# Optimization experiments

Hardware: AMD Instinct MI355X
Metric: run time of the kernel (lower is better)

## Reference

```python
import jax, jax.numpy as jnp
import numpy as np

N_NODES = 10000
N_EDGES = 160000
HID = 128
N_LAYERS = 6
N_RBF = 50
CUTOFF = 10.0
EDGE_IN = 2 * HID + N_RBF + 1  # 307


def setup_inputs() -> dict:
    key = jax.random.key(0)
    ks = jax.random.split(key, 24)
    s = 0.05
    inp = {
        'atomic_numbers': jax.random.randint(ks[0], (N_NODES,), 0, 100),
        'coords': jax.random.normal(ks[1], (N_NODES, 3), jnp.float32),
        'edge_index': jax.random.randint(ks[2], (2, N_EDGES), 0, N_NODES),
        'embed': jax.random.normal(ks[3], (100, HID), jnp.float32) * s,
        # message_net (stacked over layers)
        'mw1': jax.random.normal(ks[4], (N_LAYERS, EDGE_IN, HID), jnp.float32) * s,
        'mb1': jnp.zeros((N_LAYERS, HID), jnp.float32),
        'mw2': jax.random.normal(ks[5], (N_LAYERS, HID, HID), jnp.float32) * s,
        'mb2': jnp.zeros((N_LAYERS, HID), jnp.float32),
        # coord_net
        'cw1': jax.random.normal(ks[6], (N_LAYERS, HID, HID), jnp.float32) * s,
        'cb1': jnp.zeros((N_LAYERS, HID), jnp.float32),
        'cw2': jax.random.normal(ks[7], (N_LAYERS, HID, 1), jnp.float32) * s,
        'cb2': jnp.zeros((N_LAYERS, 1), jnp.float32),
        # feature_net
        'fw': jax.random.normal(ks[8], (N_LAYERS, 2 * HID, HID), jnp.float32) * s,
        'fb': jnp.zeros((N_LAYERS, HID), jnp.float32),
        # energy_predictor
        'ew1': jax.random.normal(ks[9], (HID, HID), jnp.float32) * s,
        'eb1': jnp.zeros((HID,), jnp.float32),
        'ew2': jax.random.normal(ks[10], (HID, 1), jnp.float32) * s,
        'eb2': jnp.zeros((1,), jnp.float32),
    }
    return inp


def _forward(atomic_numbers, coords, edge_index, embed,
             mw1, mb1, mw2, mb2, cw1, cb1, cw2, cb2, fw, fb,
             ew1, eb1, ew2, eb2):
    silu = jax.nn.silu
    n = coords.shape[0]
    row, col = edge_index[0], edge_index[1]
    feats = embed[atomic_numbers]                    # [N, H]
    # RBF edge attributes (computed once from initial coords)
    d = jnp.linalg.norm(coords[row] - coords[col], axis=-1)[:, None]  # [E,1]
    centers = jnp.linspace(0.0, CUTOFF, N_RBF)
    width = CUTOFF / N_RBF
    rbf = jnp.exp(-((d - centers) ** 2) / width)
    cut = 0.5 * (jnp.cos(jnp.pi * d / CUTOFF) + 1.0) * (d < CUTOFF).astype(d.dtype)
    edge_attr = rbf * cut                            # [E, 50]
    for l in range(N_LAYERS):
        diff = coords[row] - coords[col]             # [E, 3]
        edist = jnp.sum(diff * diff, axis=-1, keepdims=True)  # squared dist, [E,1]
        ef = jnp.concatenate([feats[row], feats[col], edist, edge_attr], axis=-1)
        m = silu(silu(ef @ mw1[l] + mb1[l]) @ mw2[l] + mb2[l])        # [E, H]
        w = silu(m @ cw1[l] + cb1[l]) @ cw2[l] + cb2[l]               # [E, 1]
        coords = coords.at[row].add(w * diff)                         # equivariant coord update
        agg = jax.ops.segment_sum(m, row, num_segments=n)             # [N, H]
        feats = silu(jnp.concatenate([feats, agg], axis=-1) @ fw[l] + fb[l])
    atom_e = silu(feats @ ew1 + eb1) @ ew2 + eb2     # [N, 1]
    return jnp.sum(atom_e)


def reference(atomic_numbers, coords, edge_index, embed,
              mw1, mb1, mw2, mb2, cw1, cb1, cw2, cb2, fw, fb,
              ew1, eb1, ew2, eb2):
    return _forward(atomic_numbers, coords, edge_index, embed,
                    mw1, mb1, mw2, mb2, cw1, cb1, cw2, cb2, fw, fb,
                    ew1, eb1, ew2, eb2)
```

## Files before the change

kernel.cpp:

```cpp
#include <hip/hip_runtime.h>
#include <math.h>

#define N_NODES  10000
#define N_EDGES  160000
#define HID      128
#define N_LAYERS 6
#define N_RBF    50
#define EDGE_IN  307
#define KP1      320
#define M_TILE   64
#define N_TILES  (N_EDGES / M_TILE)

typedef short bf16x8 __attribute__((ext_vector_type(8)));
typedef float f32x4  __attribute__((ext_vector_type(4)));

__device__ __forceinline__ float silu_f(float x) {
    return x / (1.0f + __expf(-x));
}
__device__ __forceinline__ short f2bf(float f) {
    union { float f; unsigned u; } v; v.f = f;
    unsigned r = v.u + 0x7FFFu + ((v.u >> 16) & 1u);
    return (short)(r >> 16);
}
__device__ __forceinline__ float bf2f(unsigned short s) {
    union { float f; unsigned u; } v; v.u = ((unsigned)s) << 16;
    return v.f;
}


__global__ void init_feats_kernel(const int* __restrict__ an,
                                  const float* __restrict__ embed,
                                  short* __restrict__ featsB) {
    int idx = blockIdx.x * blockDim.x + threadIdx.x;
    if (idx < N_NODES * HID) {
        int i = idx >> 7, j = idx & 127;
        featsB[idx] = f2bf(embed[an[i] * HID + j]);
    }
}

__global__ void hist_kernel(const int* __restrict__ row, int* __restrict__ cnt) {
    int e = blockIdx.x * blockDim.x + threadIdx.x;
    if (e < N_EDGES) atomicAdd(&cnt[row[e]], 1);
}

__global__ void scan_kernel(const int* __restrict__ cnt, int* __restrict__ cursor) {
    __shared__ int buf[256];
    __shared__ int carry;
    int tid = threadIdx.x;
    if (tid == 0) carry = 0;
    __syncthreads();
    for (int base = 0; base < N_NODES; base += 256) {
        int v = (base + tid < N_NODES) ? cnt[base + tid] : 0;
        buf[tid] = v;
        __syncthreads();
        for (int off = 1; off < 256; off <<= 1) {
            int x = (tid >= off) ? buf[tid - off] : 0;
            __syncthreads();
            buf[tid] += x;
            __syncthreads();
        }
        int excl = buf[tid] - v + carry;
        if (base + tid < N_NODES) cursor[base + tid] = excl;
        int tot = buf[255];
        __syncthreads();
        if (tid == 0) carry += tot;
        __syncthreads();
    }
}

__global__ void scatter_kernel(const int* __restrict__ row, int* __restrict__ cursor,
                               int* __restrict__ sorted) {
    int e = blockIdx.x * blockDim.x + threadIdx.x;
    if (e < N_EDGES) {
        int p = atomicAdd(&cursor[row[e]], 1);
        sorted[p] = e;
    }
}

__global__ void edgegeom_kernel(const int* __restrict__ sorted,
                                const int* __restrict__ erow, const int* __restrict__ ecol,
                                const float* __restrict__ coords,
                                float* __restrict__ d0, float* __restrict__ cut0) {
    int p = blockIdx.x * 256 + threadIdx.x;
    if (p < N_EDGES) {
        int e = sorted[p];
        int r = erow[e], c = ecol[e];
        float dx = coords[3*r]   - coords[3*c];
        float dy = coords[3*r+1] - coords[3*c+1];
        float dz = coords[3*r+2] - coords[3*c+2];
        float d = sqrtf(dx*dx + dy*dy + dz*dz);
        d0[p] = d;
        cut0[p] = (d < 10.0f) ? 0.5f * (__cosf(0.31415926535f * d) + 1.0f) : 0.0f;
    }
}

#define WT_L (40960 + 16384 + 16384 + 32768)
__global__ void wtrans_kernel(const float* __restrict__ mw1, const float* __restrict__ mw2,
                              const float* __restrict__ cw1, const float* __restrict__ fw,
                              short* __restrict__ wtm1, short* __restrict__ wtm2,
                              short* __restrict__ wtc1, short* __restrict__ wtf) {
    int idx = blockIdx.x * blockDim.x + threadIdx.x;
    if (idx >= N_LAYERS * WT_L) return;
    int l = idx / WT_L;
    int r = idx - l * WT_L;
    if (r < 40960) {
        int n = r / KP1, k = r - n * KP1;
        float v = (k < EDGE_IN) ? mw1[(size_t)l * EDGE_IN * HID + (size_t)k * HID + n] : 0.f;
        wtm1[(size_t)l * 40960 + r] = f2bf(v);
    } else if ((r -= 40960) < 16384) {
        int n = r >> 7, k = r & 127;
        wtm2[(size_t)l * 16384 + r] = f2bf(mw2[(size_t)l * HID * HID + (size_t)k * HID + n]);
    } else if ((r -= 16384) < 16384) {
        int n = r >> 7, k = r & 127;
        wtc1[(size_t)l * 16384 + r] = f2bf(cw1[(size_t)l * HID * HID + (size_t)k * HID + n]);
    } else {
        r -= 16384;
        int n = r >> 8, k = r & 255;
        wtf[(size_t)l * 32768 + r] = f2bf(fw[(size_t)l * 2 * HID * HID + (size_t)k * HID + n]);
    }
}


#define SMEM_BYTES 18432

__global__ __launch_bounds__(256) void edge_kernel(
    const int* __restrict__ sorted,
    const int* __restrict__ erow, const int* __restrict__ ecol,
    const float* __restrict__ coords, float* __restrict__ coords_next,
    const short* __restrict__ featsB,
    const float* __restrict__ d0g, const float* __restrict__ cut0g,
    const short* __restrict__ wtm1, const float* __restrict__ mb1,
    const short* __restrict__ wtm2, const float* __restrict__ mb2,
    const short* __restrict__ wtc1, const float* __restrict__ cb1,
    const float* __restrict__ cw2, const float* __restrict__ cb2,
    float* __restrict__ agg)
{
    __shared__ char  smem[SMEM_BYTES];
    __shared__ int   srow[M_TILE];
    __shared__ int   scol[M_TILE];
    __shared__ float sdiff[M_TILE][3];
    __shared__ float sdist[M_TILE], sd0[M_TILE], scut[M_TILE], sW[M_TILE];
    __shared__ float sWp[M_TILE][4];
    __shared__ float sB1[HID], sB2[HID], sC1[HID], sV[HID];

    short (*sA)[64][72] = (short (*)[64][72])smem;
    short (*sH)[136]    = (short (*)[136])smem;

    const int tid = threadIdx.x;
    const int p0 = blockIdx.x * M_TILE;
    const int wave = tid >> 6, lane = tid & 63, quad = lane >> 4, lm = lane & 15;
    const int el = tid >> 2, kq = (tid & 3) * 16;
    const int colA = wave * 32 + lm, colB = colA + 16;

    if (tid < M_TILE) {
        int e = sorted[p0 + tid];
        int r = erow[e], c = ecol[e];
        srow[tid] = r; scol[tid] = c;
        float dx = coords[3*r]   - coords[3*c];
        float dy = coords[3*r+1] - coords[3*c+1];
        float dz = coords[3*r+2] - coords[3*c+2];
        sdiff[tid][0] = dx; sdiff[tid][1] = dy; sdiff[tid][2] = dz;
        sdist[tid] = dx*dx + dy*dy + dz*dz;
        sd0[tid]  = d0g[p0 + tid];
        scut[tid] = cut0g[p0 + tid];
    }
    if (tid < HID) {
        sB1[tid] = mb1[tid]; sB2[tid] = mb2[tid];
        sC1[tid] = cb1[tid]; sV[tid]  = cw2[tid];
    }
    const float cb2v = cb2[0];
    __syncthreads();

    f32x4 acc[4][2];
    #pragma unroll
    for (int mt = 0; mt < 4; ++mt) { acc[mt][0] = (f32x4)0.f; acc[mt][1] = (f32x4)0.f; }

    bf16x8 bwb[2][2][2];
    {
        int node = srow[el];
        const bf16x8* src = (const bf16x8*)&featsB[(size_t)node * HID + kq];
        bf16x8 a0 = src[0], a1 = src[1];
        #pragma unroll
        for (int h = 0; h < 2; ++h) {
            bwb[0][h][0] = *(const bf16x8*)&wtm1[(size_t)colA * KP1 + h * 32 + quad * 8];
            bwb[0][h][1] = *(const bf16x8*)&wtm1[(size_t)colB * KP1 + h * 32 + quad * 8];
        }
        *(bf16x8*)&sA[0][el][kq]     = a0;
        *(bf16x8*)&sA[0][el][kq + 8] = a1;
    }
    __syncthreads();
    #pragma unroll
    for (int c = 0; c < 5; ++c) {
        bf16x8 a0, a1;
        if (c < 3) {
            int node = (c + 1 < 2) ? srow[el] : scol[el];
            const bf16x8* src =
                (const bf16x8*)&featsB[(size_t)node * HID + ((c + 1) & 1) * 64 + kq];
            a0 = src[0]; a1 = src[1];
        } else if (c == 3) {
            float dv = sd0[el], ct = scut[el], ds2 = sdist[el];
            #pragma unroll
            for (int j = 0; j < 8; ++j) {
                int k = 256 + kq + j;
                float v = 0.f;
                if (k == 256) v = ds2;
                else if (k < EDGE_IN) {
                    float cen = (float)(k - 257) * (10.0f / 49.0f);
                    float t = dv - cen;
                    v = __expf(-t * t * 5.0f) * ct;
                }
                a0[j] = f2bf(v);
            }
            #pragma unroll
            for (int j = 0; j < 8; ++j) {
                int k = 264 + kq + j;
                float v = 0.f;
                if (k < EDGE_IN) {
                    float cen = (float)(k - 257) * (10.0f / 49.0f);
                    float t = dv - cen;
                    v = __expf(-t * t * 5.0f) * ct;
                }
                a1[j] = f2bf(v);
            }
        }
        if (c < 4) {
            int k1 = (c + 1) * 64;
            #pragma unroll
            for (int h = 0; h < 2; ++h) {
                bwb[(c + 1) & 1][h][0] = *(const bf16x8*)&wtm1[(size_t)colA * KP1 + k1 + h * 32 + quad * 8];
                bwb[(c + 1) & 1][h][1] = *(const bf16x8*)&wtm1[(size_t)colB * KP1 + k1 + h * 32 + quad * 8];
            }
        }
        #pragma unroll
        for (int h = 0; h < 2; ++h) {
            bf16x8 af[4];
            #pragma unroll
            for (int mt = 0; mt < 4; ++mt)
                af[mt] = *(bf16x8*)&sA[c & 1][mt * 16 + lm][h * 32 + quad * 8];
            #pragma unroll
            for (int nb = 0; nb < 2; ++nb)
                #pragma unroll
                for (int mt = 0; mt < 4; ++mt)
                    acc[mt][nb] = __builtin_amdgcn_mfma_f32_16x16x32_bf16(
                        af[mt], bwb[c & 1][h][nb], acc[mt][nb], 0, 0, 0);
        }
        if (c < 4) {
            *(bf16x8*)&sA[(c + 1) & 1][el][kq]     = a0;
            *(bf16x8*)&sA[(c + 1) & 1][el][kq + 8] = a1;
        }
        __syncthreads();
    }

    bf16x8 bw2[4][2];
    #pragma unroll
    for (int ks = 0; ks < 4; ++ks) {
        bw2[ks][0] = *(const bf16x8*)&wtm2[(size_t)colA * HID + ks * 32 + quad * 8];
        bw2[ks][1] = *(const bf16x8*)&wtm2[(size_t)colB * HID + ks * 32 + quad * 8];
    }

    #pragma unroll
    for (int nb = 0; nb < 2; ++nb) {
        int col = wave * 32 + nb * 16 + lm;
        float b = sB1[col];
        #pragma unroll
        for (int mt = 0; mt < 4; ++mt) {
            #pragma unroll
            for (int r = 0; r < 4; ++r)
                sH[mt * 16 + quad * 4 + r][col] = f2bf(silu_f(acc[mt][nb][r] + b));
            acc[mt][nb] = (f32x4)0.f;
        }
    }
    __syncthreads();

    #pragma unroll
    for (int ks = 0; ks < 4; ++ks) {
        bf16x8 af[4];
        #pragma unroll
        for (int mt = 0; mt < 4; ++mt)
            af[mt] = *(bf16x8*)&sH[mt * 16 + lm][ks * 32 + quad * 8];
        #pragma unroll
        for (int nb = 0; nb < 2; ++nb)
            #pragma unroll
            for (int mt = 0; mt < 4; ++mt)
                acc[mt][nb] = __builtin_amdgcn_mfma_f32_16x16x32_bf16(
                    af[mt], bw2[ks][nb], acc[mt][nb], 0, 0, 0);
    }
    bf16x8 bw3[4][2];
    #pragma unroll
    for (int ks = 0; ks < 4; ++ks) {
        bw3[ks][0] = *(const bf16x8*)&wtc1[(size_t)colA * HID + ks * 32 + quad * 8];
        bw3[ks][1] = *(const bf16x8*)&wtc1[(size_t)colB * HID + ks * 32 + quad * 8];
    }
    __syncthreads();
    #pragma unroll
    for (int nb = 0; nb < 2; ++nb) {
        int col = wave * 32 + nb * 16 + lm;
        float b = sB2[col];
        #pragma unroll
        for (int mt = 0; mt < 4; ++mt) {
            float g = 0.f;
            #pragma unroll
            for (int r = 0; r < 4; ++r) {
                int row = mt * 16 + quad * 4 + r;
                float mv = silu_f(acc[mt][nb][r] + b);
                sH[row][col] = f2bf(mv);
                g += mv;
                if (r == 3 || srow[row + 1] != srow[row]) {
                    atomicAdd(&agg[(size_t)srow[row] * HID + col], g);
                    g = 0.f;
                }
            }
            acc[mt][nb] = (f32x4)0.f;
        }
    }
    __syncthreads();

    #pragma unroll
    for (int ks = 0; ks < 4; ++ks) {
        bf16x8 af[4];
        #pragma unroll
        for (int mt = 0; mt < 4; ++mt)
            af[mt] = *(bf16x8*)&sH[mt * 16 + lm][ks * 32 + quad * 8];
        #pragma unroll
        for (int nb = 0; nb < 2; ++nb)
            #pragma unroll
            for (int mt = 0; mt < 4; ++mt)
                acc[mt][nb] = __builtin_amdgcn_mfma_f32_16x16x32_bf16(
                    af[mt], bw3[ks][nb], acc[mt][nb], 0, 0, 0);
    }
    {
        float wp[4][4];
        #pragma unroll
        for (int mt = 0; mt < 4; ++mt)
            #pragma unroll
            for (int r = 0; r < 4; ++r) wp[mt][r] = 0.f;
        #pragma unroll
        for (int nb = 0; nb < 2; ++nb) {
            int col = wave * 32 + nb * 16 + lm;
            float b = sC1[col], vv = sV[col];
            #pragma unroll
            for (int mt = 0; mt < 4; ++mt)
                #pragma unroll
                for (int r = 0; r < 4; ++r)
                    wp[mt][r] += silu_f(acc[mt][nb][r] + b) * vv;
        }
        #pragma unroll
        for (int mt = 0; mt < 4; ++mt)
            #pragma unroll
            for (int r = 0; r < 4; ++r) {
                float v = wp[mt][r];
                v += __shfl_xor(v, 1); v += __shfl_xor(v, 2);
                v += __shfl_xor(v, 4); v += __shfl_xor(v, 8);
                if (lm == 0) sWp[mt * 16 + quad * 4 + r][wave] = v;
            }
    }
    __syncthreads();
    if (tid < M_TILE)
        sW[tid] = cb2v + sWp[tid][0] + sWp[tid][1] + sWp[tid][2] + sWp[tid][3];
    __syncthreads();
    if (tid < M_TILE) {
        bool leader = (tid == 0) || (srow[tid] != srow[tid - 1]);
        if (leader) {
            int rr = srow[tid];
            float ax = 0.f, ay = 0.f, az = 0.f;
            for (int k = tid; k < M_TILE && srow[k] == rr; ++k) {
                ax += sW[k] * sdiff[k][0];
                ay += sW[k] * sdiff[k][1];
                az += sW[k] * sdiff[k][2];
            }
            atomicAdd(&coords_next[3*rr+0], ax);
            atomicAdd(&coords_next[3*rr+1], ay);
            atomicAdd(&coords_next[3*rr+2], az);
        }
    }
}

__global__ __launch_bounds__(256) void node_kernel(
    const short* __restrict__ featsB, const float* __restrict__ agg,
    const short* __restrict__ wtf, const float* __restrict__ fb,
    short* __restrict__ outB)
{
    __shared__ short sA[32][72];
    __shared__ short sO[32][136];
    __shared__ float sFb[HID];

    const int tid = threadIdx.x;
    const int n0 = blockIdx.x * 32;
    const int wave = tid >> 6, lane = tid & 63, quad = lane >> 4, lm = lane & 15;

    if (tid < HID) sFb[tid] = fb[tid];

    f32x4 acc[2][2];
    acc[0][0] = (f32x4)0.f; acc[0][1] = (f32x4)0.f;
    acc[1][0] = (f32x4)0.f; acc[1][1] = (f32x4)0.f;
    __syncthreads();

    for (int c = 0; c < 4; ++c) {
        int k0 = c * 64;
        bf16x8 bw[2][2];
        #pragma unroll
        for (int h = 0; h < 2; ++h) {
            int col0 = wave * 32 + lm;
            bw[h][0] = *(const bf16x8*)&wtf[(size_t)col0 * 256 + k0 + h * 32 + quad * 8];
            bw[h][1] = *(const bf16x8*)&wtf[(size_t)(col0 + 16) * 256 + k0 + h * 32 + quad * 8];
        }
        {
            int el = tid >> 3, kq = (tid & 7) * 8;
            int node = n0 + el;
            if (node < N_NODES) {
                if (c < 2) {
                    *(bf16x8*)&sA[el][kq] =
                        *(const bf16x8*)&featsB[(size_t)node * HID + k0 + kq];
                } else {
                    const float* ap = &agg[(size_t)node * HID + (k0 - 128) + kq];
                    bf16x8 v;
                    #pragma unroll
                    for (int j = 0; j < 8; ++j) v[j] = f2bf(ap[j]);
                    *(bf16x8*)&sA[el][kq] = v;
                }
            } else {
                *(bf16x8*)&sA[el][kq] = (bf16x8)0;
            }
        }
        __syncthreads();
        #pragma unroll
        for (int h = 0; h < 2; ++h) {
            bf16x8 af[2];
            af[0] = *(bf16x8*)&sA[lm][h * 32 + quad * 8];
            af[1] = *(bf16x8*)&sA[16 + lm][h * 32 + quad * 8];
            #pragma unroll
            for (int nb = 0; nb < 2; ++nb) {
                acc[0][nb] = __builtin_amdgcn_mfma_f32_16x16x32_bf16(af[0], bw[h][nb], acc[0][nb], 0, 0, 0);
                acc[1][nb] = __builtin_amdgcn_mfma_f32_16x16x32_bf16(af[1], bw[h][nb], acc[1][nb], 0, 0, 0);
            }
        }
        __syncthreads();
    }
    #pragma unroll
    for (int nb = 0; nb < 2; ++nb) {
        int col = wave * 32 + nb * 16 + lm;
        float b = sFb[col];
        #pragma unroll
        for (int mt = 0; mt < 2; ++mt)
            #pragma unroll
            for (int r = 0; r < 4; ++r)
                sO[mt * 16 + quad * 4 + r][col] = f2bf(silu_f(acc[mt][nb][r] + b));
    }
    __syncthreads();
    {
        int row = tid >> 3, ch = (tid & 7) * 8;
        int node = n0 + row;
        if (node < N_NODES) {
            *(bf16x8*)&outB[(size_t)node * HID + ch]      = *(bf16x8*)&sO[row][ch];
            *(bf16x8*)&outB[(size_t)node * HID + 64 + ch] = *(bf16x8*)&sO[row][64 + ch];
        }
    }
}

#define FMA8(r, aq) \
    acc[r][0] += (aq)*b0.x; acc[r][1] += (aq)*b0.y; acc[r][2] += (aq)*b0.z; acc[r][3] += (aq)*b0.w; \
    acc[r][4] += (aq)*b1.x; acc[r][5] += (aq)*b1.y; acc[r][6] += (aq)*b1.z; acc[r][7] += (aq)*b1.w;

__global__ __launch_bounds__(256) void energy_kernel(
    const short* __restrict__ featsB,
    const float* __restrict__ ew1, const float* __restrict__ eb1,
    const float* __restrict__ ew2, const float* __restrict__ eb2,
    float* __restrict__ out)
{
    __shared__ float sA[64][20];
    __shared__ float sB[16][HID];
    __shared__ float sV[HID];
    __shared__ float red[256];
    int tid = threadIdx.x;
    int n0 = blockIdx.x * 64;
    const int tr = tid >> 4, tc = tid & 15;
    const int r0 = tr * 4, c0 = tc * 4, c1 = c0 + 64;
    const int el = tid >> 2, kq = (tid & 3) * 4;

    if (tid < HID) sV[tid] = ew2[tid];

    float acc[4][8];
    #pragma unroll
    for (int i = 0; i < 4; i++)
        #pragma unroll
        for (int j = 0; j < 8; j++) acc[i][j] = 0.f;

    for (int kt = 0; kt < 8; ++kt) {
        int k0 = kt * 16;
        {
            int k = k0 + kq;
            int node = n0 + el;
            float4 v = make_float4(0,0,0,0);
            if (node < N_NODES) {
                const unsigned short* p = (const unsigned short*)&featsB[(size_t)node * HID + k];
                v.x = bf2f(p[0]); v.y = bf2f(p[1]); v.z = bf2f(p[2]); v.w = bf2f(p[3]);
            }
            *(float4*)&sA[el][kq] = v;
        }
        {
            int bk = tid >> 4, bj = (tid & 15) * 8;
            int k = k0 + bk;
            *(float4*)&sB[bk][bj]     = *(const float4*)&ew1[(size_t)k * HID + bj];
            *(float4*)&sB[bk][bj + 4] = *(const float4*)&ew1[(size_t)k * HID + bj + 4];
        }
        __syncthreads();
        #pragma unroll
        for (int kk4 = 0; kk4 < 4; ++kk4) {
            float4 a0 = *(const float4*)&sA[r0 + 0][kk4 * 4];
            float4 a1 = *(const float4*)&sA[r0 + 1][kk4 * 4];
            float4 a2 = *(const float4*)&sA[r0 + 2][kk4 * 4];
            float4 a3 = *(const float4*)&sA[r0 + 3][kk4 * 4];
            #pragma unroll
            for (int q = 0; q < 4; ++q) {
                int kk = kk4 * 4 + q;
                float4 b0 = *(const float4*)&sB[kk][c0];
                float4 b1 = *(const float4*)&sB[kk][c1];
                float q0 = ((const float*)&a0)[q], q1 = ((const float*)&a1)[q];
                float q2 = ((const float*)&a2)[q], q3 = ((const float*)&a3)[q];
                FMA8(0, q0) FMA8(1, q1) FMA8(2, q2) FMA8(3, q3)
            }
        }
        __syncthreads();
    }
    float part = 0.f;
    #pragma unroll
    for (int i = 0; i < 4; i++) {
        int node = n0 + r0 + i;
        if (node < N_NODES) {
            #pragma unroll
            for (int j = 0; j < 4; j++) {
                part += silu_f(acc[i][j]     + eb1[c0+j]) * sV[c0+j];
                part += silu_f(acc[i][4 + j] + eb1[c1+j]) * sV[c1+j];
            }
        }
    }
    red[tid] = part;
    __syncthreads();
    for (int s = 128; s > 0; s >>= 1) {
        if (tid < s) red[tid] += red[tid + s];
        __syncthreads();
    }
    if (tid == 0) {
        float v = red[0];
        if (blockIdx.x == 0) v += eb2[0] * (float)N_NODES;
        atomicAdd(out, v);
    }
}


extern "C" void kernel_launch(void* const* d_in, const int* in_sizes, int n_in,
                              void* d_out, int out_size, void* d_ws, size_t ws_size,
                              hipStream_t stream)
{
    const int*   an     = (const int*)  d_in[0];
    const float* coords = (const float*)d_in[1];
    const int*   ei     = (const int*)  d_in[2];
    const float* embed  = (const float*)d_in[3];
    const float* mw1 = (const float*)d_in[4];
    const float* mb1 = (const float*)d_in[5];
    const float* mw2 = (const float*)d_in[6];
    const float* mb2 = (const float*)d_in[7];
    const float* cw1 = (const float*)d_in[8];
    const float* cb1 = (const float*)d_in[9];
    const float* cw2 = (const float*)d_in[10];
    const float* cb2 = (const float*)d_in[11];
    const float* fw  = (const float*)d_in[12];
    const float* fb  = (const float*)d_in[13];
    const float* ew1 = (const float*)d_in[14];
    const float* eb1 = (const float*)d_in[15];
    const float* ew2 = (const float*)d_in[16];
    const float* eb2 = (const float*)d_in[17];
    float* out = (float*)d_out;

    char* w = (char*)d_ws;
    size_t off = 0;
    auto alloc = [&](size_t bytes) -> char* {
        char* p = w + off;
        off = (off + bytes + 511) & ~(size_t)511;
        return p;
    };
    short* featsB0 = (short*)alloc((size_t)N_NODES * HID * 2);
    short* featsB1 = (short*)alloc((size_t)N_NODES * HID * 2);
    float* agg     = (float*)alloc((size_t)N_NODES * HID * 4);
    float* cA      = (float*)alloc((size_t)N_NODES * 3 * 4);
    float* cB      = (float*)alloc((size_t)N_NODES * 3 * 4);
    float* d0      = (float*)alloc((size_t)N_EDGES * 4);
    float* cut0    = (float*)alloc((size_t)N_EDGES * 4);
    int*   sorted  = (int*)  alloc((size_t)N_EDGES * 4);
    int*   cnt     = (int*)  alloc((size_t)N_NODES * 4);
    int*   cursor  = (int*)  alloc((size_t)N_NODES * 4);
    short* wtm1    = (short*)alloc((size_t)N_LAYERS * 40960 * 2);
    short* wtm2    = (short*)alloc((size_t)N_LAYERS * 16384 * 2);
    short* wtc1    = (short*)alloc((size_t)N_LAYERS * 16384 * 2);
    short* wtf     = (short*)alloc((size_t)N_LAYERS * 32768 * 2);

    const int* erow = ei;
    const int* ecol = ei + N_EDGES;

    hipMemsetAsync(cnt, 0, (size_t)N_NODES * 4, stream);
    init_feats_kernel<<<(N_NODES * HID + 255) / 256, 256, 0, stream>>>(an, embed, featsB0);
    wtrans_kernel<<<(N_LAYERS * WT_L + 255) / 256, 256, 0, stream>>>(
        mw1, mw2, cw1, fw, wtm1, wtm2, wtc1, wtf);
    hipMemcpyAsync(cA, coords, (size_t)N_NODES * 3 * 4, hipMemcpyDeviceToDevice, stream);
    hist_kernel<<<(N_EDGES + 255) / 256, 256, 0, stream>>>(erow, cnt);
    scan_kernel<<<1, 256, 0, stream>>>(cnt, cursor);
    scatter_kernel<<<(N_EDGES + 255) / 256, 256, 0, stream>>>(erow, cursor, sorted);
    edgegeom_kernel<<<N_EDGES / 256, 256, 0, stream>>>(sorted, erow, ecol, cA, d0, cut0);

    short* fc = featsB0; short* fn = featsB1;
    float* cc = cA;      float* cn = cB;
    for (int l = 0; l < N_LAYERS; ++l) {
        hipMemsetAsync(agg, 0, (size_t)N_NODES * HID * 4, stream);
        hipMemcpyAsync(cn, cc, (size_t)N_NODES * 3 * 4, hipMemcpyDeviceToDevice, stream);
        edge_kernel<<<N_TILES, 256, 0, stream>>>(
            sorted, erow, ecol, cc, cn, fc, d0, cut0,
            wtm1 + (size_t)l * 40960, mb1 + (size_t)l * HID,
            wtm2 + (size_t)l * 16384, mb2 + (size_t)l * HID,
            wtc1 + (size_t)l * 16384, cb1 + (size_t)l * HID,
            cw2 + (size_t)l * HID,    cb2 + l, agg);
        node_kernel<<<(N_NODES + 31) / 32, 256, 0, stream>>>(
            fc, agg, wtf + (size_t)l * 32768, fb + (size_t)l * HID, fn);
        { short* t = fc; fc = fn; fn = t; }
        { float* t = cc; cc = cn; cn = t; }
    }
    hipMemsetAsync(out, 0, 4, stream);
    energy_kernel<<<(N_NODES + 63) / 64, 256, 0, stream>>>(fc, ew1, eb1, ew2, eb2, out);
}
```

Measured before the change: 786.4 us.

## Precompute per-node first-layer projections so edges gather projected features

```diff
diff --git a/kernel.cpp b/kernel.cpp
--- a/kernel.cpp
+++ b/kernel.cpp
@@ -1,4 +1,5 @@
 #include <hip/hip_runtime.h>
+#include <hip/hip_bf16.h>
 #include <math.h>
 
 #define N_NODES  10000
@@ -7,7 +8,6 @@
 #define N_LAYERS 6
 #define N_RBF    50
 #define EDGE_IN  307
-#define KP1      320
 #define M_TILE   64
 #define N_TILES  (N_EDGES / M_TILE)
 
@@ -15,7 +15,8 @@
 typedef float f32x4  __attribute__((ext_vector_type(4)));
 
 __device__ __forceinline__ float silu_f(float x) {
-    return x / (1.0f + __expf(-x));
+    float e = __expf(-x);
+    return x * __builtin_amdgcn_rcpf(1.0f + e);
 }
 __device__ __forceinline__ short f2bf(float f) {
     union { float f; unsigned u; } v; v.f = f;
@@ -25,6 +26,10 @@
 __device__ __forceinline__ float bf2f(unsigned short s) {
     union { float f; unsigned u; } v; v.u = ((unsigned)s) << 16;
     return v.f;
+}
+__device__ __forceinline__ unsigned pk_bf(float a, float b) {
+    __hip_bfloat162 h = __float22bfloat162_rn(float2{a, b});
+    unsigned u; __builtin_memcpy(&u, &h, 4); return u;
 }
 
 
@@ -94,48 +99,124 @@
     }
 }
 
-#define WT_L (40960 + 16384 + 16384 + 32768)
+#define SZ_M1E 8192
+#define SZ_P   32768
+#define SZ_M2  16384
+#define SZ_C1  16384
+#define SZ_F   32768
+#define WT_L   (SZ_M1E + SZ_P + SZ_M2 + SZ_C1 + SZ_F)
 __global__ void wtrans_kernel(const float* __restrict__ mw1, const float* __restrict__ mw2,
                               const float* __restrict__ cw1, const float* __restrict__ fw,
-                              short* __restrict__ wtm1, short* __restrict__ wtm2,
-                              short* __restrict__ wtc1, short* __restrict__ wtf) {
+                              short* __restrict__ wtm1e, short* __restrict__ wtp,
+                              short* __restrict__ wtm2, short* __restrict__ wtc1,
+                              short* __restrict__ wtf) {
     int idx = blockIdx.x * blockDim.x + threadIdx.x;
     if (idx >= N_LAYERS * WT_L) return;
     int l = idx / WT_L;
     int r = idx - l * WT_L;
-    if (r < 40960) {
-        int n = r / KP1, k = r - n * KP1;
-        float v = (k < EDGE_IN) ? mw1[(size_t)l * EDGE_IN * HID + (size_t)k * HID + n] : 0.f;
-        wtm1[(size_t)l * 40960 + r] = f2bf(v);
-    } else if ((r -= 40960) < 16384) {
+    const float* m1 = mw1 + (size_t)l * EDGE_IN * HID;
+    if (r < SZ_M1E) {
+        int n = r >> 6, k = r & 63;
+        float v = 0.f;
+        if (k == 0) v = m1[(size_t)256 * HID + n];
+        else if (k <= 50) v = m1[(size_t)(256 + k) * HID + n];
+        wtm1e[(size_t)l * SZ_M1E + r] = f2bf(v);
+    } else if ((r -= SZ_M1E) < SZ_P) {
         int n = r >> 7, k = r & 127;
-        wtm2[(size_t)l * 16384 + r] = f2bf(mw2[(size_t)l * HID * HID + (size_t)k * HID + n]);
-    } else if ((r -= 16384) < 16384) {
+        float v = (n < HID) ? m1[(size_t)k * HID + n]
+                            : m1[(size_t)(HID + k) * HID + (n - HID)];
+        wtp[(size_t)l * SZ_P + r] = f2bf(v);
+    } else if ((r -= SZ_P) < SZ_M2) {
         int n = r >> 7, k = r & 127;
-        wtc1[(size_t)l * 16384 + r] = f2bf(cw1[(size_t)l * HID * HID + (size_t)k * HID + n]);
+        wtm2[(size_t)l * SZ_M2 + r] = f2bf(mw2[(size_t)l * HID * HID + (size_t)k * HID + n]);
+    } else if ((r -= SZ_M2) < SZ_C1) {
+        int n = r >> 7, k = r & 127;
+        wtc1[(size_t)l * SZ_C1 + r] = f2bf(cw1[(size_t)l * HID * HID + (size_t)k * HID + n]);
     } else {
-        r -= 16384;
+        r -= SZ_C1;
         int n = r >> 8, k = r & 255;
-        wtf[(size_t)l * 32768 + r] = f2bf(fw[(size_t)l * 2 * HID * HID + (size_t)k * HID + n]);
-    }
-}
-
-
-#define SMEM_BYTES 18432
+        wtf[(size_t)l * SZ_F + r] = f2bf(fw[(size_t)l * 2 * HID * HID + (size_t)k * HID + n]);
+    }
+}
+
+__global__ __launch_bounds__(256) void p_kernel(
+    const short* __restrict__ featsB, const short* __restrict__ wtp,
+    short* __restrict__ Pg)
+{
+    __shared__ short sA[32][136];
+    const int tid = threadIdx.x;
+    const int n0 = blockIdx.x * 32;
+    const int wave = tid >> 6, lane = tid & 63, quad = lane >> 4, lm = lane & 15;
+
+    {
+        int el = tid >> 3, kq = (tid & 7) * 16;
+        int node = n0 + el;
+        if (node < N_NODES) {
+            const bf16x8* src = (const bf16x8*)&featsB[(size_t)node * HID + kq];
+            *(bf16x8*)&sA[el][kq]     = src[0];
+            *(bf16x8*)&sA[el][kq + 8] = src[1];
+        } else {
+            *(bf16x8*)&sA[el][kq]     = (bf16x8)0;
+            *(bf16x8*)&sA[el][kq + 8] = (bf16x8)0;
+        }
+    }
+    bf16x8 bw[4][4];
+    #pragma unroll
+    for (int h = 0; h < 4; ++h)
+        #pragma unroll
+        for (int nb = 0; nb < 4; ++nb) {
+            int col = wave * 64 + nb * 16 + lm;
+            bw[h][nb] = *(const bf16x8*)&wtp[(size_t)col * HID + h * 32 + quad * 8];
+        }
+    __syncthreads();
+
+    f32x4 acc[2][4];
+    #pragma unroll
+    for (int mt = 0; mt < 2; ++mt)
+        #pragma unroll
+        for (int nb = 0; nb < 4; ++nb) acc[mt][nb] = (f32x4)0.f;
+
+    #pragma unroll
+    for (int h = 0; h < 4; ++h) {
+        bf16x8 af[2];
+        af[0] = *(bf16x8*)&sA[lm][h * 32 + quad * 8];
+        af[1] = *(bf16x8*)&sA[16 + lm][h * 32 + quad * 8];
+        #pragma unroll
+        for (int nb = 0; nb < 4; ++nb) {
+            acc[0][nb] = __builtin_amdgcn_mfma_f32_16x16x32_bf16(af[0], bw[h][nb], acc[0][nb], 0, 0, 0);
+            acc[1][nb] = __builtin_amdgcn_mfma_f32_16x16x32_bf16(af[1], bw[h][nb], acc[1][nb], 0, 0, 0);
+        }
+    }
+    #pragma unroll
+    for (int mt = 0; mt < 2; ++mt)
+        #pragma unroll
+        for (int r = 0; r < 4; ++r) {
+            int node = n0 + mt * 16 + quad * 4 + r;
+            if (node < N_NODES) {
+                #pragma unroll
+                for (int nb = 0; nb < 4; ++nb) {
+                    int col = wave * 64 + nb * 16 + lm;
+                    Pg[(size_t)node * 256 + col] = f2bf(acc[mt][nb][r]);
+                }
+            }
+        }
+}
+
 
 __global__ __launch_bounds__(256) void edge_kernel(
     const int* __restrict__ sorted,
     const int* __restrict__ erow, const int* __restrict__ ecol,
     const float* __restrict__ coords, float* __restrict__ coords_next,
-    const short* __restrict__ featsB,
+    const short* __restrict__ Pg,
     const float* __restrict__ d0g, const float* __restrict__ cut0g,
-    const short* __restrict__ wtm1, const float* __restrict__ mb1,
+    const short* __restrict__ wtm1e, const float* __restrict__ mb1,
     const short* __restrict__ wtm2, const float* __restrict__ mb2,
     const short* __restrict__ wtc1, const float* __restrict__ cb1,
     const float* __restrict__ cw2, const float* __restrict__ cb2,
     float* __restrict__ agg)
 {
-    __shared__ char  smem[SMEM_BYTES];
+    __shared__ short sH[M_TILE][136];
+    __shared__ short sA[M_TILE][72];
     __shared__ int   srow[M_TILE];
     __shared__ int   scol[M_TILE];
     __shared__ float sdiff[M_TILE][3];
@@ -143,13 +224,9 @@
     __shared__ float sWp[M_TILE][4];
     __shared__ float sB1[HID], sB2[HID], sC1[HID], sV[HID];
 
-    short (*sA)[64][72] = (short (*)[64][72])smem;
-    short (*sH)[136]    = (short (*)[136])smem;
-
     const int tid = threadIdx.x;
     const int p0 = blockIdx.x * M_TILE;
     const int wave = tid >> 6, lane = tid & 63, quad = lane >> 4, lm = lane & 15;
-    const int el = tid >> 2, kq = (tid & 3) * 16;
     const int colA = wave * 32 + lm, colB = colA + 16;
 
     if (tid < M_TILE) {
@@ -171,104 +248,92 @@
     const float cb2v = cb2[0];
     __syncthreads();
 
-    f32x4 acc[4][2];
-    #pragma unroll
-    for (int mt = 0; mt < 4; ++mt) { acc[mt][0] = (f32x4)0.f; acc[mt][1] = (f32x4)0.f; }
-
-    bf16x8 bwb[2][2][2];
     {
-        int node = srow[el];
-        const bf16x8* src = (const bf16x8*)&featsB[(size_t)node * HID + kq];
-        bf16x8 a0 = src[0], a1 = src[1];
-        #pragma unroll
-        for (int h = 0; h < 2; ++h) {
-            bwb[0][h][0] = *(const bf16x8*)&wtm1[(size_t)colA * KP1 + h * 32 + quad * 8];
-            bwb[0][h][1] = *(const bf16x8*)&wtm1[(size_t)colB * KP1 + h * 32 + quad * 8];
-        }
-        *(bf16x8*)&sA[0][el][kq]     = a0;
-        *(bf16x8*)&sA[0][el][kq + 8] = a1;
-    }
-    __syncthreads();
-    #pragma unroll
-    for (int c = 0; c < 5; ++c) {
-        bf16x8 a0, a1;
-        if (c < 3) {
-            int node = (c + 1 < 2) ? srow[el] : scol[el];
-            const bf16x8* src =
-                (const bf16x8*)&featsB[(size_t)node * HID + ((c + 1) & 1) * 64 + kq];
-            a0 = src[0]; a1 = src[1];
-        } else if (c == 3) {
-            float dv = sd0[el], ct = scut[el], ds2 = sdist[el];
+        int el = tid >> 2, kq = (tid & 3) * 32;
+        const short* p1 = &Pg[(size_t)srow[el] * 256 + kq];
+        const short* p2 = &Pg[(size_t)scol[el] * 256 + 128 + kq];
+        #pragma unroll
+        for (int g = 0; g < 4; ++g) {
+            bf16x8 a = *(const bf16x8*)&p1[g * 8];
+            bf16x8 b = *(const bf16x8*)&p2[g * 8];
+            bf16x8 o;
+            #pragma unroll
+            for (int j = 0; j < 8; j += 2) {
+                float s0 = bf2f((unsigned short)a[j])     + bf2f((unsigned short)b[j]);
+                float s1 = bf2f((unsigned short)a[j + 1]) + bf2f((unsigned short)b[j + 1]);
+                unsigned u = pk_bf(s0, s1);
+                o[j] = (short)(u & 0xFFFF); o[j + 1] = (short)(u >> 16);
+            }
+            *(bf16x8*)&sH[el][kq + g * 8] = o;
+        }
+    }
+    {
+        int el = tid >> 2, kq = (tid & 3) * 16;
+        float dv = sd0[el], ct = scut[el], ds2 = sdist[el];
+        #pragma unroll
+        for (int g = 0; g < 2; ++g) {
+            bf16x8 v;
             #pragma unroll
             for (int j = 0; j < 8; ++j) {
-                int k = 256 + kq + j;
-                float v = 0.f;
-                if (k == 256) v = ds2;
-                else if (k < EDGE_IN) {
-                    float cen = (float)(k - 257) * (10.0f / 49.0f);
+                int k = kq + g * 8 + j;
+                float val = 0.f;
+                if (k == 0) val = ds2;
+                else if (k <= N_RBF) {
+                    float cen = (float)(k - 1) * (10.0f / 49.0f);
                     float t = dv - cen;
-                    v = __expf(-t * t * 5.0f) * ct;
+                    val = __expf(-t * t * 5.0f) * ct;
                 }
-                a0[j] = f2bf(v);
-            }
-            #pragma unroll
-            for (int j = 0; j < 8; ++j) {
-                int k = 264 + kq + j;
-                float v = 0.f;
-                if (k < EDGE_IN) {
-                    float cen = (float)(k - 257) * (10.0f / 49.0f);
-                    float t = dv - cen;
-                    v = __expf(-t * t * 5.0f) * ct;
-                }
-                a1[j] = f2bf(v);
-            }
-        }
-        if (c < 4) {
-            int k1 = (c + 1) * 64;
-            #pragma unroll
-            for (int h = 0; h < 2; ++h) {
-                bwb[(c + 1) & 1][h][0] = *(const bf16x8*)&wtm1[(size_t)colA * KP1 + k1 + h * 32 + quad * 8];
-                bwb[(c + 1) & 1][h][1] = *(const bf16x8*)&wtm1[(size_t)colB * KP1 + k1 + h * 32 + quad * 8];
-            }
-        }
-        #pragma unroll
-        for (int h = 0; h < 2; ++h) {
-            bf16x8 af[4];
-            #pragma unroll
-            for (int mt = 0; mt < 4; ++mt)
-                af[mt] = *(bf16x8*)&sA[c & 1][mt * 16 + lm][h * 32 + quad * 8];
-            #pragma unroll
-            for (int nb = 0; nb < 2; ++nb)
-                #pragma unroll
-                for (int mt = 0; mt < 4; ++mt)
-                    acc[mt][nb] = __builtin_amdgcn_mfma_f32_16x16x32_bf16(
-                        af[mt], bwb[c & 1][h][nb], acc[mt][nb], 0, 0, 0);
-        }
-        if (c < 4) {
-            *(bf16x8*)&sA[(c + 1) & 1][el][kq]     = a0;
-            *(bf16x8*)&sA[(c + 1) & 1][el][kq + 8] = a1;
-        }
-        __syncthreads();
-    }
-
+                v[j] = f2bf(val);
+            }
+            *(bf16x8*)&sA[el][kq + g * 8] = v;
+        }
+    }
+    bf16x8 bw1[2][2];
+    #pragma unroll
+    for (int h = 0; h < 2; ++h) {
+        bw1[h][0] = *(const bf16x8*)&wtm1e[(size_t)colA * 64 + h * 32 + quad * 8];
+        bw1[h][1] = *(const bf16x8*)&wtm1e[(size_t)colB * 64 + h * 32 + quad * 8];
+    }
     bf16x8 bw2[4][2];
     #pragma unroll
     for (int ks = 0; ks < 4; ++ks) {
         bw2[ks][0] = *(const bf16x8*)&wtm2[(size_t)colA * HID + ks * 32 + quad * 8];
         bw2[ks][1] = *(const bf16x8*)&wtm2[(size_t)colB * HID + ks * 32 + quad * 8];
     }
-
-    #pragma unroll
-    for (int nb = 0; nb < 2; ++nb) {
-        int col = wave * 32 + nb * 16 + lm;
-        float b = sB1[col];
-        #pragma unroll
-        for (int mt = 0; mt < 4; ++mt) {
-            #pragma unroll
-            for (int r = 0; r < 4; ++r)
-                sH[mt * 16 + quad * 4 + r][col] = f2bf(silu_f(acc[mt][nb][r] + b));
-            acc[mt][nb] = (f32x4)0.f;
-        }
+    __syncthreads();
+
+    f32x4 acc[4][2];
+    #pragma unroll
+    for (int mt = 0; mt < 4; ++mt) { acc[mt][0] = (f32x4)0.f; acc[mt][1] = (f32x4)0.f; }
+
+    #pragma unroll
+    for (int h = 0; h < 2; ++h) {
+        bf16x8 af[4];
+        #pragma unroll
+        for (int mt = 0; mt < 4; ++mt)
+            af[mt] = *(bf16x8*)&sA[mt * 16 + lm][h * 32 + quad * 8];
+        #pragma unroll
+        for (int nb = 0; nb < 2; ++nb)
+            #pragma unroll
+            for (int mt = 0; mt < 4; ++mt)
+                acc[mt][nb] = __builtin_amdgcn_mfma_f32_16x16x32_bf16(
+                    af[mt], bw1[h][nb], acc[mt][nb], 0, 0, 0);
+    }
+    #pragma unroll
+    for (int mt = 0; mt < 4; ++mt) {
+        float bA = sB1[colA], bB = sB1[colB];
+        #pragma unroll
+        for (int r = 0; r < 4; ++r) {
+            int row = mt * 16 + quad * 4 + r;
+            float pA = bf2f((unsigned short)sH[row][colA]);
+            float pB = bf2f((unsigned short)sH[row][colB]);
+            float hA = silu_f(acc[mt][0][r] + pA + bA);
+            float hB = silu_f(acc[mt][1][r] + pB + bB);
+            unsigned u = pk_bf(hA, hB);
+            sH[row][colA] = (short)(u & 0xFFFF);
+            sH[row][colB] = (short)(u >> 16);
+        }
+        acc[mt][0] = (f32x4)0.f; acc[mt][1] = (f32x4)0.f;
     }
     __syncthreads();
 
@@ -415,7 +480,10 @@
                     const float* ap = &agg[(size_t)node * HID + (k0 - 128) + kq];
                     bf16x8 v;
                     #pragma unroll
-                    for (int j = 0; j < 8; ++j) v[j] = f2bf(ap[j]);
+                    for (int j = 0; j < 8; j += 2) {
+                        unsigned u = pk_bf(ap[j], ap[j + 1]);
+                        v[j] = (short)(u & 0xFFFF); v[j + 1] = (short)(u >> 16);
+                    }
                     *(bf16x8*)&sA[el][kq] = v;
                 }
             } else {
@@ -437,14 +505,17 @@
         __syncthreads();
     }
     #pragma unroll
-    for (int nb = 0; nb < 2; ++nb) {
-        int col = wave * 32 + nb * 16 + lm;
-        float b = sFb[col];
-        #pragma unroll
-        for (int mt = 0; mt < 2; ++mt)
-            #pragma unroll
-            for (int r = 0; r < 4; ++r)
-                sO[mt * 16 + quad * 4 + r][col] = f2bf(silu_f(acc[mt][nb][r] + b));
+    for (int mt = 0; mt < 2; ++mt) {
+        float bA = sFb[wave * 32 + lm], bB = sFb[wave * 32 + 16 + lm];
+        #pragma unroll
+        for (int r = 0; r < 4; ++r) {
+            int row = mt * 16 + quad * 4 + r;
+            float hA = silu_f(acc[mt][0][r] + bA);
+            float hB = silu_f(acc[mt][1][r] + bB);
+            unsigned u = pk_bf(hA, hB);
+            sO[row][wave * 32 + lm]      = (short)(u & 0xFFFF);
+            sO[row][wave * 32 + 16 + lm] = (short)(u >> 16);
+        }
     }
     __syncthreads();
     {
@@ -581,6 +652,7 @@
     };
     short* featsB0 = (short*)alloc((size_t)N_NODES * HID * 2);
     short* featsB1 = (short*)alloc((size_t)N_NODES * HID * 2);
+    short* Pg      = (short*)alloc((size_t)N_NODES * 256 * 2);
     float* agg     = (float*)alloc((size_t)N_NODES * HID * 4);
     float* cA      = (float*)alloc((size_t)N_NODES * 3 * 4);
     float* cB      = (float*)alloc((size_t)N_NODES * 3 * 4);
@@ -589,10 +661,11 @@
     int*   sorted  = (int*)  alloc((size_t)N_EDGES * 4);
     int*   cnt     = (int*)  alloc((size_t)N_NODES * 4);
     int*   cursor  = (int*)  alloc((size_t)N_NODES * 4);
-    short* wtm1    = (short*)alloc((size_t)N_LAYERS * 40960 * 2);
-    short* wtm2    = (short*)alloc((size_t)N_LAYERS * 16384 * 2);
-    short* wtc1    = (short*)alloc((size_t)N_LAYERS * 16384 * 2);
-    short* wtf     = (short*)alloc((size_t)N_LAYERS * 32768 * 2);
+    short* wtm1e   = (short*)alloc((size_t)N_LAYERS * SZ_M1E * 2);
+    short* wtp     = (short*)alloc((size_t)N_LAYERS * SZ_P * 2);
+    short* wtm2    = (short*)alloc((size_t)N_LAYERS * SZ_M2 * 2);
+    short* wtc1    = (short*)alloc((size_t)N_LAYERS * SZ_C1 * 2);
+    short* wtf     = (short*)alloc((size_t)N_LAYERS * SZ_F * 2);
 
     const int* erow = ei;
     const int* ecol = ei + N_EDGES;
@@ -600,12 +673,13 @@
     hipMemsetAsync(cnt, 0, (size_t)N_NODES * 4, stream);
     init_feats_kernel<<<(N_NODES * HID + 255) / 256, 256, 0, stream>>>(an, embed, featsB0);
     wtrans_kernel<<<(N_LAYERS * WT_L + 255) / 256, 256, 0, stream>>>(
-        mw1, mw2, cw1, fw, wtm1, wtm2, wtc1, wtf);
+        mw1, mw2, cw1, fw, wtm1e, wtp, wtm2, wtc1, wtf);
     hipMemcpyAsync(cA, coords, (size_t)N_NODES * 3 * 4, hipMemcpyDeviceToDevice, stream);
     hist_kernel<<<(N_EDGES + 255) / 256, 256, 0, stream>>>(erow, cnt);
     scan_kernel<<<1, 256, 0, stream>>>(cnt, cursor);
     scatter_kernel<<<(N_EDGES + 255) / 256, 256, 0, stream>>>(erow, cursor, sorted);
     edgegeom_kernel<<<N_EDGES / 256, 256, 0, stream>>>(sorted, erow, ecol, cA, d0, cut0);
+    p_kernel<<<(N_NODES + 31) / 32, 256, 0, stream>>>(featsB0, wtp, Pg);
 
     short* fc = featsB0; short* fn = featsB1;
     float* cc = cA;      float* cn = cB;
@@ -613,15 +687,18 @@
         hipMemsetAsync(agg, 0, (size_t)N_NODES * HID * 4, stream);
         hipMemcpyAsync(cn, cc, (size_t)N_NODES * 3 * 4, hipMemcpyDeviceToDevice, stream);
         edge_kernel<<<N_TILES, 256, 0, stream>>>(
-            sorted, erow, ecol, cc, cn, fc, d0, cut0,
-            wtm1 + (size_t)l * 40960, mb1 + (size_t)l * HID,
-            wtm2 + (size_t)l * 16384, mb2 + (size_t)l * HID,
-            wtc1 + (size_t)l * 16384, cb1 + (size_t)l * HID,
-            cw2 + (size_t)l * HID,    cb2 + l, agg);
+            sorted, erow, ecol, cc, cn, Pg, d0, cut0,
+            wtm1e + (size_t)l * SZ_M1E, mb1 + (size_t)l * HID,
+            wtm2  + (size_t)l * SZ_M2,  mb2 + (size_t)l * HID,
+            wtc1  + (size_t)l * SZ_C1,  cb1 + (size_t)l * HID,
+            cw2 + (size_t)l * HID,      cb2 + l, agg);
         node_kernel<<<(N_NODES + 31) / 32, 256, 0, stream>>>(
-            fc, agg, wtf + (size_t)l * 32768, fb + (size_t)l * HID, fn);
+            fc, agg, wtf + (size_t)l * SZ_F, fb + (size_t)l * HID, fn);
         { short* t = fc; fc = fn; fn = t; }
         { float* t = cc; cc = cn; cn = t; }
+        if (l + 1 < N_LAYERS)
+            p_kernel<<<(N_NODES + 31) / 32, 256, 0, stream>>>(
+                fc, wtp + (size_t)(l + 1) * SZ_P, Pg);
     }
     hipMemsetAsync(out, 0, 4, stream);
     energy_kernel<<<(N_NODES + 63) / 64, 256, 0, stream>>>(fc, ew1, eb1, ew2, eb2, out);
```

Result: faster. 748.3 us (-4.8%).
